# Kernel optimization log

Hardware: AMD Instinct MI355X
Metric: run time of the kernel (lower is better)

Reference implementation:

```python
import jax, jax.numpy as jnp
import numpy as np

N = 50000      # nodes
E = 400000     # edges (before self-loops)
IN = 128       # input feature dim
HID = 32       # out_channels per head
HEADS = 12
NC = 2         # num_classes
SLOPE = 0.2    # GATv2 leaky_relu negative slope


def setup_inputs() -> dict:
    key = jax.random.key(0)
    ks = jax.random.split(key, 24)
    f32 = jnp.float32
    def nrm(k, shape, s=0.1):
        return jax.random.normal(k, shape, dtype=f32) * s
    inp = {}
    inp["x"] = jax.random.normal(ks[0], (N, IN), dtype=f32)
    inp["edge_index"] = jax.random.randint(ks[1], (2, E), 0, N, dtype=jnp.int32)
    # GATv2 layer 0: in=IN, layer 1: in=HID; both heads=HEADS, out=HID, concat=False
    dims = [IN, HID]
    i = 2
    for l, d in enumerate(dims):
        inp[f"Wl{l}"] = nrm(ks[i], (d, HEADS * HID)); i += 1
        inp[f"bl{l}"] = jnp.zeros((HEADS * HID,), f32)
        inp[f"Wr{l}"] = nrm(ks[i], (d, HEADS * HID)); i += 1
        inp[f"br{l}"] = jnp.zeros((HEADS * HID,), f32)
        inp[f"att{l}"] = nrm(ks[i], (HEADS, HID)); i += 1
        inp[f"bias{l}"] = jnp.zeros((HID,), f32)
    # output GATv2Conv(HID, NC): heads=1, concat=True
    inp["Wlo"] = nrm(ks[i], (HID, NC)); i += 1
    inp["blo"] = jnp.zeros((NC,), f32)
    inp["Wro"] = nrm(ks[i], (HID, NC)); i += 1
    inp["bro"] = jnp.zeros((NC,), f32)
    inp["atto"] = nrm(ks[i], (1, NC)); i += 1
    inp["biaso"] = jnp.zeros((NC,), f32)
    return inp


def gatv2_conv(x, src, dst, Wl, bl, Wr, br, att, bias, heads, out_ch, concat):
    """PyG GATv2Conv (share_weights=False, self-loops pre-appended, eval mode)."""
    n = x.shape[0]
    xl = (x @ Wl + bl).reshape(n, heads, out_ch)   # source transform
    xr = (x @ Wr + br).reshape(n, heads, out_ch)   # target transform
    # per-edge attention: e_ij = att . leaky_relu(xl_j + xr_i)
    h = jax.nn.leaky_relu(xl[src] + xr[dst], SLOPE)            # [E, H, C]
    logits = jnp.einsum('ehc,hc->eh', h, att)                   # [E, H]
    # segment softmax over incoming edges per destination node
    m = jax.ops.segment_max(logits, dst, num_segments=n)        # [N, H]
    a = jnp.exp(logits - m[dst])
    denom = jax.ops.segment_sum(a, dst, num_segments=n)         # [N, H]
    alpha = a / (denom[dst] + 1e-16)                            # [E, H]
    out = jax.ops.segment_sum(xl[src] * alpha[..., None], dst, num_segments=n)
    out = out.reshape(n, heads * out_ch) if concat else out.mean(axis=1)
    return out + bias


def reference(x, edge_index, Wl0, bl0, Wr0, br0, att0, bias0,
              Wl1, bl1, Wr1, br1, att1, bias1,
              Wlo, blo, Wro, bro, atto, biaso):
    n = x.shape[0]
    loop = jnp.arange(n, dtype=edge_index.dtype)
    src = jnp.concatenate([edge_index[0], loop])  # add self-loops (PyG default)
    dst = jnp.concatenate([edge_index[1], loop])
    h = gatv2_conv(x, src, dst, Wl0, bl0, Wr0, br0, att0, bias0, HEADS, HID, False)
    h = jax.nn.elu(h)
    h = gatv2_conv(h, src, dst, Wl1, bl1, Wr1, br1, att1, bias1, HEADS, HID, False)
    h = jax.nn.elu(h)
    out = gatv2_conv(h, src, dst, Wlo, blo, Wro, bro, atto, biaso, 1, NC, True)
    return out
```

## Files before the change

### kernel.cpp

```cpp
#include <hip/hip_runtime.h>
#include <hip/hip_fp16.h>
#include <math.h>

#define IN_DIM 128
#define HID 32
#define HEADS 12
#define FDIM (HEADS*HID)
#define SLOPE 0.2f
#define LOG2E 1.44269504f

typedef __attribute__((ext_vector_type(8))) short short8;
typedef __attribute__((ext_vector_type(4))) float float4v;
typedef __attribute__((ext_vector_type(4))) float f32x4;
typedef _Float16 hv2 __attribute__((ext_vector_type(2)));

__device__ __forceinline__ float dot2acc(hv2 a, hv2 b, float c) {
#if __has_builtin(__builtin_amdgcn_fdot2)
    return __builtin_amdgcn_fdot2(a, b, c, false);
#else
    return c + (float)a.x * (float)b.x + (float)a.y * (float)b.y;
#endif
}

__device__ __forceinline__ float exp2h(float x) {
#if __has_builtin(__builtin_amdgcn_exp2f)
    return __builtin_amdgcn_exp2f(x);
#else
    return exp2f(x);
#endif
}

__device__ __forceinline__ float fma_mix_lo(hv2 x, float a, float c) {
    float d;
    asm("v_fma_mix_f32 %0, %1, %2, %3 op_sel_hi:[1,0,0]"
        : "=v"(d) : "v"(x), "v"(a), "v"(c));
    return d;
}
__device__ __forceinline__ float fma_mix_hi(hv2 x, float a, float c) {
    float d;
    asm("v_fma_mix_f32 %0, %1, %2, %3 op_sel:[1,0,0] op_sel_hi:[1,0,0]"
        : "=v"(d) : "v"(x), "v"(a), "v"(c));
    return d;
}

__device__ __forceinline__ void async_cp16(const void* g, void* l) {
    __builtin_amdgcn_global_load_lds(
        (const __attribute__((address_space(1))) void*)g,
        (__attribute__((address_space(3))) void*)l, 16, 0, 0);
}


__global__ __launch_bounds__(256) void scan_partial_kernel(const int* __restrict__ cnt,
                                                           int* __restrict__ partials, int n) {
    int i = blockIdx.x * 256 + threadIdx.x;
    int v = (i < n) ? cnt[i] + 1 : 0;
#pragma unroll
    for (int off = 1; off < 64; off <<= 1) v += __shfl_xor(v, off);
    __shared__ int sh[4];
    if ((threadIdx.x & 63) == 0) sh[threadIdx.x >> 6] = v;
    __syncthreads();
    if (threadIdx.x == 0) partials[blockIdx.x] = sh[0] + sh[1] + sh[2] + sh[3];
}

__global__ __launch_bounds__(256) void scan_final_kernel(const int* __restrict__ cnt,
                                                         const int* __restrict__ partials,
                                                         int* __restrict__ start,
                                                         int* __restrict__ cursor,
                                                         int* __restrict__ srcs,
                                                         int* __restrict__ srcsOff, int n) {
    __shared__ int sh[256];
    __shared__ int ps[4];
    int t = threadIdx.x;
    int pv = 0;
    for (int j = t; j < blockIdx.x; j += 256) pv += partials[j];
#pragma unroll
    for (int off = 1; off < 64; off <<= 1) pv += __shfl_xor(pv, off);
    if ((t & 63) == 0) ps[t >> 6] = pv;

    int i = blockIdx.x * 256 + t;
    int v = (i < n) ? cnt[i] + 1 : 0;
    sh[t] = v;
    __syncthreads();
    int base = ps[0] + ps[1] + ps[2] + ps[3];
    for (int off = 1; off < 256; off <<= 1) {
        int u = (t >= off) ? sh[t - off] : 0;
        __syncthreads();
        sh[t] += u;
        __syncthreads();
    }
    int ex = sh[t] - v + base;
    if (i < n) {
        start[i] = ex;
        cursor[i] = ex;
        int slot = ex + v - 1;
        srcs[slot] = i;
        srcsOff[slot] = i * (FDIM * 2);
        if (i == n - 1) start[n] = ex + v;
    }
}

__global__ void scatter_kernel(const int* __restrict__ src, const int* __restrict__ dst,
                               int* __restrict__ cursor, int* __restrict__ srcs,
                               int* __restrict__ srcsOff, int E) {
    int e = blockIdx.x * blockDim.x + threadIdx.x;
    if (e < E) {
        int d = dst[e];
        int pos = atomicAdd(&cursor[d], 1);
        int s = src[e];
        srcs[pos] = s;
        srcsOff[pos] = s * (FDIM * 2);
    }
}


__device__ __forceinline__ unsigned int bf16_rne(float f) {
    unsigned int u = __float_as_uint(f);
    return (u + 0x7FFFu + ((u >> 16) & 1u)) >> 16;
}


__global__ void prep_conv(const float* __restrict__ x, short* __restrict__ Ah,
                          short* __restrict__ Al, int total4, int convBlocks,
                          const float* __restrict__ Wl0, const float* __restrict__ Wr0,
                          const float* __restrict__ Wl1, const float* __restrict__ Wr1,
                          const float* __restrict__ a0, const float* __restrict__ a1,
                          short* __restrict__ Bl0h, short* __restrict__ Bl0l,
                          short* __restrict__ Br0h, short* __restrict__ Br0l,
                          short* __restrict__ Bl1h, short* __restrict__ Bl1l,
                          short* __restrict__ Br1h, short* __restrict__ Br1l,
                          _Float16* __restrict__ attH,
                          const int* __restrict__ edst, int* __restrict__ cnt, int E) {
    if (blockIdx.x < (unsigned)convBlocks) {
        int i = blockIdx.x * 256 + threadIdx.x;
        if (i >= total4) return;
        float4 v = ((const float4*)x)[i];
        float fs[4] = {v.x, v.y, v.z, v.w};
        unsigned int hb[4], lb[4];
#pragma unroll
        for (int t = 0; t < 4; t++) {
            hb[t] = bf16_rne(fs[t]);
            lb[t] = bf16_rne(fs[t] - __uint_as_float(hb[t] << 16));
        }
        uint2 hp, lp;
        hp.x = hb[0] | (hb[1] << 16); hp.y = hb[2] | (hb[3] << 16);
        lp.x = lb[0] | (lb[1] << 16); lp.y = lb[2] | (lb[3] << 16);
        ((uint2*)Ah)[i] = hp;
        ((uint2*)Al)[i] = lp;
        return;
    }
    if (blockIdx.x < (unsigned)(convBlocks + 243)) {
        int idx = (blockIdx.x - convBlocks) * 256 + threadIdx.x;
        if (idx < 49152) {
            int k = idx / 384, n = idx - k * 384;
            float w1 = Wl0[idx], w2 = Wr0[idx];
            unsigned int h1 = bf16_rne(w1);
            unsigned int l1 = bf16_rne(w1 - __uint_as_float(h1 << 16));
            unsigned int h2 = bf16_rne(w2);
            unsigned int l2 = bf16_rne(w2 - __uint_as_float(h2 << 16));
            Bl0h[n * 128 + k] = (short)h1;  Bl0l[n * 128 + k] = (short)l1;
            Br0h[n * 128 + k] = (short)h2;  Br0l[n * 128 + k] = (short)l2;
        } else if (idx < 61440) {
            int i2 = idx - 49152;
            int k = i2 / 384, n = i2 - k * 384;
            float w1 = Wl1[i2], w2 = Wr1[i2];
            unsigned int h1 = bf16_rne(w1);
            unsigned int l1 = bf16_rne(w1 - __uint_as_float(h1 << 16));
            unsigned int h2 = bf16_rne(w2);
            unsigned int l2 = bf16_rne(w2 - __uint_as_float(h2 << 16));
            Bl1h[n * 32 + k] = (short)h1;  Bl1l[n * 32 + k] = (short)l1;
            Br1h[n * 32 + k] = (short)h2;  Br1l[n * 32 + k] = (short)l2;
        } else if (idx < 62208) {
            int i2 = idx - 61440;
            attH[i2] = (_Float16)(((i2 < 384) ? a0[i2] : a1[i2 - 384]) * LOG2E);
        }
        return;
    }
    int e = (blockIdx.x - convBlocks - 243) * 256 + threadIdx.x;
    if (e < E) atomicAdd(&cnt[edst[e]], 1);
}


__global__ __launch_bounds__(256) void gemm_pair_async(
    const short* __restrict__ Ahi, const short* __restrict__ Alo,
    const short* __restrict__ B1h, const short* __restrict__ B1l,
    const float* __restrict__ bias1, __half* __restrict__ C1,
    const short* __restrict__ B2h, const short* __restrict__ B2l,
    const float* __restrict__ bias2, __half* __restrict__ C2,
    int M, int K, int nwg) {
    __shared__ __align__(16) unsigned char smem[32768];
    int tid = threadIdx.x;
    int lane = tid & 63;
    int wave = tid >> 6;
    int wm = wave & 1, wn = wave >> 1;

    int bid = blockIdx.x;
    int q8 = nwg >> 3, r8 = nwg & 7;
    int xcd = bid & 7, within = bid >> 3;
    int wgid = (xcd < r8 ? xcd * (q8 + 1) : r8 * (q8 + 1) + (xcd - r8) * q8) + within;
    int bx = wgid / 6;
    int by = wgid - bx * 6;

    int rowBase = bx * 128;
    bool second = by >= 3;
    int colBase = (by - (second ? 3 : 0)) * 128;
    const short* Bh  = second ? B2h : B1h;
    const short* Bl  = second ? B2l : B1l;
    const float* bias = second ? bias2 : bias1;
    __half*      C    = second ? C2 : C1;

    const short8* AsHi = (const short8*)smem;
    const short8* AsLo = (const short8*)(smem + 8192);
    const short8* BsHi = (const short8*)(smem + 16384);
    const short8* BsLo = (const short8*)(smem + 24576);

    const short* gsrc[8];
    void* ldst[8];
#pragma unroll
    for (int q = 0; q < 8; q++) {
        int t  = (q & 1) * 4 + wave;
        int rc = t * 16 + (lane & 15);
        int ko = (lane >> 4) * 8;
        const short* base = (q < 2) ? Ahi : (q < 4) ? Alo : (q < 6) ? Bh : Bl;
        int rb = (q < 4) ? rowBase : colBase;
        gsrc[q] = base + (long)(rb + rc) * K + ko;
        ldst[q] = (void*)(smem + q * 4096 + wave * 1024);
    }

    float4v acc[4][4];
#pragma unroll
    for (int i = 0; i < 4; i++)
#pragma unroll
        for (int j = 0; j < 4; j++) acc[i][j] = (float4v){0.f, 0.f, 0.f, 0.f};

    for (int kt = 0; kt < K; kt += 32) {
#pragma unroll
        for (int q = 0; q < 8; q++) {
            async_cp16(gsrc[q], ldst[q]);
            gsrc[q] += 32;
        }
        __syncthreads();

        short8 ah[4], al[4], bh[4], blv[4];
#pragma unroll
        for (int i = 0; i < 4; i++) {
            ah[i]  = AsHi[(wm * 4 + i) * 64 + lane];
            al[i]  = AsLo[(wm * 4 + i) * 64 + lane];
            bh[i]  = BsHi[(wn * 4 + i) * 64 + lane];
            blv[i] = BsLo[(wn * 4 + i) * 64 + lane];
        }
#pragma unroll
        for (int i = 0; i < 4; i++)
#pragma unroll
            for (int j = 0; j < 4; j++) {
                acc[i][j] = __builtin_amdgcn_mfma_f32_16x16x32_bf16(ah[i], bh[j],  acc[i][j], 0, 0, 0);
                acc[i][j] = __builtin_amdgcn_mfma_f32_16x16x32_bf16(ah[i], blv[j], acc[i][j], 0, 0, 0);
                acc[i][j] = __builtin_amdgcn_mfma_f32_16x16x32_bf16(al[i], bh[j],  acc[i][j], 0, 0, 0);
            }
        __syncthreads();
    }

    float* Ct = (float*)smem;
    int cq = lane >> 4, cn = lane & 15;
#pragma unroll
    for (int pp = 0; pp < 4; pp++) {
        int ph = pp >> 1, rr = pp & 1;
        if (wm == ph) {
#pragma unroll
            for (int ii = 0; ii < 2; ii++) {
                int i = 2 * rr + ii;
#pragma unroll
                for (int j = 0; j < 4; j++) {
                    int lrb = ii * 16 + cq * 4;
                    int lc = wn * 64 + j * 16 + cn;
#pragma unroll
                    for (int r = 0; r < 4; r++)
                        Ct[(lrb + r) * 132 + lc] = acc[i][j][r];
                }
            }
        }
        __syncthreads();
#pragma unroll
        for (int k = 0; k < 2; k++) {
            int o = k * 256 + tid;
            int lrb = o >> 4;
            int oc = (o & 15) << 3;
            int gr = rowBase + ph * 64 + rr * 32 + lrb;
            if (gr < M) {
                float4 f0 = *(float4*)&Ct[lrb * 132 + oc];
                float4 f1 = *(float4*)&Ct[lrb * 132 + oc + 4];
                int gc = colBase + oc;
                float4 b0 = *(const float4*)(bias + gc);
                float4 b1 = *(const float4*)(bias + gc + 4);
                __half2 p0 = __floats2half2_rn(f0.x + b0.x, f0.y + b0.y);
                __half2 p1 = __floats2half2_rn(f0.z + b0.z, f0.w + b0.w);
                __half2 p2 = __floats2half2_rn(f1.x + b1.x, f1.y + b1.y);
                __half2 p3 = __floats2half2_rn(f1.z + b1.z, f1.w + b1.w);
                uint4 ov;
                ov.x = *(unsigned int*)&p0;
                ov.y = *(unsigned int*)&p1;
                ov.z = *(unsigned int*)&p2;
                ov.w = *(unsigned int*)&p3;
                *(uint4*)(C + (size_t)gr * FDIM + gc) = ov;
            }
        }
        __syncthreads();
    }
}


__global__ __launch_bounds__(64) void agg_kernel(const __half* __restrict__ xl,
                                                 const __half* __restrict__ xr,
                                                 const _Float16* __restrict__ att_h,
                                                 const float* __restrict__ bias,
                                                 const int* __restrict__ start,
                                                 const int* __restrict__ srcsOff,
                                                 short* __restrict__ houtHi,
                                                 short* __restrict__ houtLo,
                                                 const float* __restrict__ Wl,
                                                 const float* __restrict__ bl,
                                                 const float* __restrict__ Wr,
                                                 const float* __restrict__ br,
                                                 float* __restrict__ xloB,
                                                 float* __restrict__ xroB, int N) {
    int node = blockIdx.x;
    if (node >= N) return;
    int lane = threadIdx.x & 63;
    int hl = lane & 31;
    int half_ = lane >> 5;
    int cb = hl << 3;

    long nodeOff = (long)node * (FDIM * 2);
    hv2 xr2[6], at2[6];
    f32x4 acc[3];
    float s[3];
#pragma unroll
    for (int c = 0; c < 3; c++) {
        uint2 ur = *(const uint2*)((const char*)xr + nodeOff + c * 256 + cb);
        xr2[2*c]   = __builtin_bit_cast(hv2, ur.x);
        xr2[2*c+1] = __builtin_bit_cast(hv2, ur.y);
        uint2 ua = *(const uint2*)((const char*)att_h + c * 256 + cb);
        at2[2*c]   = __builtin_bit_cast(hv2, ua.x);
        at2[2*c+1] = __builtin_bit_cast(hv2, ua.y);
        acc[c] = (f32x4){0.f, 0.f, 0.f, 0.f};
        s[c] = 0.f;
    }
    const hv2 sl2 = {(_Float16)SLOPE, (_Float16)SLOPE};
    const char* xlb = (const char*)xl + cb;

    int e0 = start[node], e1 = start[node + 1];
    int b = e0;

    int offA0 = 0, offA1 = 0;
    if (b + 4 <= e1) {
        offA0 = srcsOff[b + half_];
        offA1 = srcsOff[b + 2 + half_];
    }
    for (; b + 4 <= e1; b += 4) {
        int offN0 = srcsOff[b + 4 + half_];
        int offN1 = srcsOff[b + 6 + half_];
        hv2 xa[2][6];
        {
            const char* base0 = xlb + (long)offA0;
            uint2 u0 = *(const uint2*)(base0);
            uint2 u1 = *(const uint2*)(base0 + 256);
            uint2 u2 = *(const uint2*)(base0 + 512);
            xa[0][0] = __builtin_bit_cast(hv2, u0.x); xa[0][1] = __builtin_bit_cast(hv2, u0.y);
            xa[0][2] = __builtin_bit_cast(hv2, u1.x); xa[0][3] = __builtin_bit_cast(hv2, u1.y);
            xa[0][4] = __builtin_bit_cast(hv2, u2.x); xa[0][5] = __builtin_bit_cast(hv2, u2.y);
            const char* base1 = xlb + (long)offA1;
            uint2 v0 = *(const uint2*)(base1);
            uint2 v1 = *(const uint2*)(base1 + 256);
            uint2 v2 = *(const uint2*)(base1 + 512);
            xa[1][0] = __builtin_bit_cast(hv2, v0.x); xa[1][1] = __builtin_bit_cast(hv2, v0.y);
            xa[1][2] = __builtin_bit_cast(hv2, v1.x); xa[1][3] = __builtin_bit_cast(hv2, v1.y);
            xa[1][4] = __builtin_bit_cast(hv2, v2.x); xa[1][5] = __builtin_bit_cast(hv2, v2.y);
        }
#pragma unroll
        for (int p = 0; p < 2; p++) {
            float pc[3];
#pragma unroll
            for (int c = 0; c < 3; c++) {
                hv2 t0 = xa[p][2*c]   + xr2[2*c];
                hv2 t1 = xa[p][2*c+1] + xr2[2*c+1];
                t0 = __builtin_elementwise_max(t0, t0 * sl2);
                t1 = __builtin_elementwise_max(t1, t1 * sl2);
                pc[c] = dot2acc(t1, at2[2*c+1], dot2acc(t0, at2[2*c], 0.f));
            }
#pragma unroll
            for (int st = 1; st <= 4; st <<= 1) {
                pc[0] += __shfl_xor(pc[0], st);
                pc[1] += __shfl_xor(pc[1], st);
                pc[2] += __shfl_xor(pc[2], st);
            }
#pragma unroll
            for (int c = 0; c < 3; c++) {
                float a = exp2h(pc[c]);
                s[c] += a;
                acc[c].x = fma_mix_lo(xa[p][2*c],   a, acc[c].x);
                acc[c].y = fma_mix_hi(xa[p][2*c],   a, acc[c].y);
                acc[c].z = fma_mix_lo(xa[p][2*c+1], a, acc[c].z);
                acc[c].w = fma_mix_hi(xa[p][2*c+1], a, acc[c].w);
            }
        }
        offA0 = offN0;
        offA1 = offN1;
    }

    if (b < e1) {
        hv2 xa[2][6];
        float mask[2];
#pragma unroll
        for (int p = 0; p < 2; p++) {
            int myIdx = b + p * 2 + half_;
            int ic = min(myIdx, e1 - 1);
            mask[p] = (myIdx < e1) ? 0.f : -1e30f;
            const char* base = xlb + (long)srcsOff[ic];
            uint2 u0 = *(const uint2*)(base);
            uint2 u1 = *(const uint2*)(base + 256);
            uint2 u2 = *(const uint2*)(base + 512);
            xa[p][0] = __builtin_bit_cast(hv2, u0.x); xa[p][1] = __builtin_bit_cast(hv2, u0.y);
            xa[p][2] = __builtin_bit_cast(hv2, u1.x); xa[p][3] = __builtin_bit_cast(hv2, u1.y);
            xa[p][4] = __builtin_bit_cast(hv2, u2.x); xa[p][5] = __builtin_bit_cast(hv2, u2.y);
        }
#pragma unroll
        for (int p = 0; p < 2; p++) {
            float pc[3];
#pragma unroll
            for (int c = 0; c < 3; c++) {
                hv2 t0 = xa[p][2*c]   + xr2[2*c];
                hv2 t1 = xa[p][2*c+1] + xr2[2*c+1];
                t0 = __builtin_elementwise_max(t0, t0 * sl2);
                t1 = __builtin_elementwise_max(t1, t1 * sl2);
                pc[c] = dot2acc(t1, at2[2*c+1], dot2acc(t0, at2[2*c], 0.f));
            }
#pragma unroll
            for (int st = 1; st <= 4; st <<= 1) {
                pc[0] += __shfl_xor(pc[0], st);
                pc[1] += __shfl_xor(pc[1], st);
                pc[2] += __shfl_xor(pc[2], st);
            }
#pragma unroll
            for (int c = 0; c < 3; c++) {
                float a = exp2h(pc[c] + mask[p]);
                s[c] += a;
                acc[c].x = fma_mix_lo(xa[p][2*c],   a, acc[c].x);
                acc[c].y = fma_mix_hi(xa[p][2*c],   a, acc[c].y);
                acc[c].z = fma_mix_lo(xa[p][2*c+1], a, acc[c].z);
                acc[c].w = fma_mix_hi(xa[p][2*c+1], a, acc[c].w);
            }
        }
    }

#pragma unroll
    for (int c = 0; c < 3; c++) {
        acc[c].x += __shfl_xor(acc[c].x, 32);
        acc[c].y += __shfl_xor(acc[c].y, 32);
        acc[c].z += __shfl_xor(acc[c].z, 32);
        acc[c].w += __shfl_xor(acc[c].w, 32);
        s[c] += __shfl_xor(s[c], 32);
    }
    f32x4 v[3];
#pragma unroll
    for (int c = 0; c < 3; c++) {
        float inv = 1.f / (s[c] + 1e-16f);
        f32x4 iv = {inv, inv, inv, inv};
        v[c] = acc[c] * iv;
    }
#pragma unroll
    for (int st = 8; st <= 16; st <<= 1) {
#pragma unroll
        for (int c = 0; c < 3; c++) {
            v[c].x += __shfl_xor(v[c].x, st);
            v[c].y += __shfl_xor(v[c].y, st);
            v[c].z += __shfl_xor(v[c].z, st);
            v[c].w += __shfl_xor(v[c].w, st);
        }
    }
    if (lane < 8) {
        f32x4 b4 = *(const f32x4*)(bias + (hl << 2));
        f32x4 o = (v[0] + v[1] + v[2]) * (f32x4){1.f/12.f, 1.f/12.f, 1.f/12.f, 1.f/12.f} + b4;
        o.x = o.x > 0.f ? o.x : expm1f(o.x);
        o.y = o.y > 0.f ? o.y : expm1f(o.y);
        o.z = o.z > 0.f ? o.z : expm1f(o.z);
        o.w = o.w > 0.f ? o.w : expm1f(o.w);
        if (houtHi) {
            float fs[4] = {o.x, o.y, o.z, o.w};
            unsigned int hb[4], lb[4];
#pragma unroll
            for (int t = 0; t < 4; t++) {
                hb[t] = bf16_rne(fs[t]);
                lb[t] = bf16_rne(fs[t] - __uint_as_float(hb[t] << 16));
            }
            uint2 hp, lp;
            hp.x = hb[0] | (hb[1] << 16); hp.y = hb[2] | (hb[3] << 16);
            lp.x = lb[0] | (lb[1] << 16); lp.y = lb[2] | (lb[3] << 16);
            *(uint2*)(houtHi + (size_t)node * 32 + (hl << 2)) = hp;
            *(uint2*)(houtLo + (size_t)node * 32 + (hl << 2)) = lp;
        }
        if (Wl) {
            f32x4 wl0 = *(const f32x4*)(Wl + (hl << 3));
            f32x4 wl1 = *(const f32x4*)(Wl + (hl << 3) + 4);
            f32x4 wr0 = *(const f32x4*)(Wr + (hl << 3));
            f32x4 wr1 = *(const f32x4*)(Wr + (hl << 3) + 4);
            float l0 = o.x * wl0.x + o.y * wl0.z + o.z * wl1.x + o.w * wl1.z;
            float l1 = o.x * wl0.y + o.y * wl0.w + o.z * wl1.y + o.w * wl1.w;
            float r0 = o.x * wr0.x + o.y * wr0.z + o.z * wr1.x + o.w * wr1.z;
            float r1 = o.x * wr0.y + o.y * wr0.w + o.z * wr1.y + o.w * wr1.w;
#pragma unroll
            for (int st = 1; st <= 4; st <<= 1) {
                l0 += __shfl_xor(l0, st); l1 += __shfl_xor(l1, st);
                r0 += __shfl_xor(r0, st); r1 += __shfl_xor(r1, st);
            }
            if (hl == 0) {
                xloB[2 * node]     = l0 + bl[0];
                xloB[2 * node + 1] = l1 + bl[1];
                xroB[2 * node]     = r0 + br[0];
                xroB[2 * node + 1] = r1 + br[1];
            }
        }
    }
}


__global__ __launch_bounds__(256) void out_agg_kernel(const float* __restrict__ xlo,
                                                      const float* __restrict__ xro,
                                                      const float* __restrict__ atto,
                                                      const float* __restrict__ biaso,
                                                      const int* __restrict__ start,
                                                      const int* __restrict__ srcs,
                                                      float* __restrict__ out, int N) {
    int g = (blockIdx.x * blockDim.x + threadIdx.x) >> 3;
    int j = threadIdx.x & 7;
    if (g >= N) return;
    float a0 = atto[0] * LOG2E, a1 = atto[1] * LOG2E;
    float xr0 = xro[2 * g], xr1 = xro[2 * g + 1];
    float s = 0.f, acc0 = 0.f, acc1 = 0.f;
    int e0 = start[g], e1 = start[g + 1];
    for (int idx = e0 + j; idx < e1; idx += 8) {
        int jj = srcs[idx];
        float x0 = xlo[2 * jj], x1 = xlo[2 * jj + 1];
        float t0 = x0 + xr0, t1 = x1 + xr1;
        t0 = fmaxf(t0, SLOPE * t0);
        t1 = fmaxf(t1, SLOPE * t1);
        float a = exp2h(a0 * t0 + a1 * t1);
        s += a;
        acc0 = fmaf(a, x0, acc0);
        acc1 = fmaf(a, x1, acc1);
    }
#pragma unroll
    for (int st = 1; st <= 4; st <<= 1) {
        s    += __shfl_xor(s, st);
        acc0 += __shfl_xor(acc0, st);
        acc1 += __shfl_xor(acc1, st);
    }
    if (j == 0) {
        float inv = 1.0f / (s + 1e-16f);
        out[2 * g]     = acc0 * inv + biaso[0];
        out[2 * g + 1] = acc1 * inv + biaso[1];
    }
}


extern "C" void kernel_launch(void* const* d_in, const int* in_sizes, int n_in,
                              void* d_out, int out_size, void* d_ws, size_t ws_size,
                              hipStream_t stream) {
    const float* x    = (const float*)d_in[0];
    const int*   ei   = (const int*)d_in[1];
    const float* Wl0  = (const float*)d_in[2];
    const float* bl0  = (const float*)d_in[3];
    const float* Wr0  = (const float*)d_in[4];
    const float* br0  = (const float*)d_in[5];
    const float* att0 = (const float*)d_in[6];
    const float* bias0= (const float*)d_in[7];
    const float* Wl1  = (const float*)d_in[8];
    const float* bl1  = (const float*)d_in[9];
    const float* Wr1  = (const float*)d_in[10];
    const float* br1  = (const float*)d_in[11];
    const float* att1 = (const float*)d_in[12];
    const float* bias1= (const float*)d_in[13];
    const float* Wlo  = (const float*)d_in[14];
    const float* blo  = (const float*)d_in[15];
    const float* Wro  = (const float*)d_in[16];
    const float* bro  = (const float*)d_in[17];
    const float* atto = (const float*)d_in[18];
    const float* biaso= (const float*)d_in[19];

    const int N = in_sizes[0] / IN_DIM;
    const int E = in_sizes[1] / 2;

    char* ws = (char*)d_ws;
    size_t off = 0;
    auto take = [&](size_t bytes) -> char* {
        char* p = ws + off;
        off += (bytes + 255) & ~(size_t)255;
        return p;
    };
    __half* xlf = (__half*)take((size_t)N * FDIM * 2);
    __half* xrf = (__half*)take((size_t)N * FDIM * 2);
    float* xloB = (float*)take((size_t)N * 2 * 4);
    float* xroB = (float*)take((size_t)N * 2 * 4);
    int* cnt    = (int*)take((size_t)N * 4);
    int* startA = (int*)take((size_t)(N + 1) * 4);
    int* cursor = (int*)take((size_t)N * 4);
    int* srcs   = (int*)take((size_t)(E + N) * 4);
    int* srcsOff= (int*)take((size_t)(E + N) * 4);
    int  nb     = (N + 255) / 256;
    int* partials = (int*)take((size_t)nb * 4);
    short* Bl0h = (short*)take((size_t)FDIM * IN_DIM * 2);
    short* Bl0l = (short*)take((size_t)FDIM * IN_DIM * 2);
    short* Br0h = (short*)take((size_t)FDIM * IN_DIM * 2);
    short* Br0l = (short*)take((size_t)FDIM * IN_DIM * 2);
    short* Bl1h = (short*)take((size_t)FDIM * HID * 2);
    short* Bl1l = (short*)take((size_t)FDIM * HID * 2);
    short* Br1h = (short*)take((size_t)FDIM * HID * 2);
    short* Br1l = (short*)take((size_t)FDIM * HID * 2);
    short* xh   = (short*)take((size_t)N * IN_DIM * 2);
    short* xlo_ = (short*)take((size_t)N * IN_DIM * 2);
    short* h0h  = (short*)take((size_t)N * HID * 2);
    short* h0l  = (short*)take((size_t)N * HID * 2);
    _Float16* attH = (_Float16*)take((size_t)768 * 2);
    (void)take(32768);

    const int* esrc = ei;
    const int* edst = ei + E;

    hipMemsetAsync(cnt, 0, (size_t)N * 4, stream);

    int total4 = N * IN_DIM / 4;
    int convBlocks = (total4 + 255) / 256;
    int histBlocks = (E + 255) / 256;
    prep_conv<<<convBlocks + 243 + histBlocks, 256, 0, stream>>>(
        x, xh, xlo_, total4, convBlocks,
        Wl0, Wr0, Wl1, Wr1, att0, att1,
        Bl0h, Bl0l, Br0h, Br0l,
        Bl1h, Bl1l, Br1h, Br1l, attH,
        edst, cnt, E);

    scan_partial_kernel<<<nb, 256, 0, stream>>>(cnt, partials, N);
    scan_final_kernel<<<nb, 256, 0, stream>>>(cnt, partials, startA, cursor, srcs, srcsOff, N);
    scatter_kernel<<<(E + 255) / 256, 256, 0, stream>>>(esrc, edst, cursor, srcs, srcsOff, E);

    int gx = (N + 127) / 128;
    int nwg = gx * 6;
    gemm_pair_async<<<nwg, 256, 0, stream>>>(xh, xlo_, Bl0h, Bl0l, bl0, xlf, Br0h, Br0l, br0, xrf, N, IN_DIM, nwg);
    agg_kernel<<<N, 64, 0, stream>>>(xlf, xrf, attH, bias0, startA, srcsOff,
                                     h0h, h0l, nullptr, nullptr, nullptr, nullptr,
                                     nullptr, nullptr, N);
    gemm_pair_async<<<nwg, 256, 0, stream>>>(h0h, h0l, Bl1h, Bl1l, bl1, xlf, Br1h, Br1l, br1, xrf, N, HID, nwg);
    agg_kernel<<<N, 64, 0, stream>>>(xlf, xrf, attH + 384, bias1, startA, srcsOff,
                                     nullptr, nullptr, Wlo, blo, Wro, bro,
                                     xloB, xroB, N);
    out_agg_kernel<<<((size_t)N * 8 + 255) / 256, 256, 0, stream>>>(xloB, xroB, atto, biaso, startA, srcs, (float*)d_out, N);
}
```

Baseline: 361.3 us.

## Software-pipeline edge gathers with double-buffered feature registers in aggregation loop

Restructures the per-node edge aggregation loop so the xl feature gather for the next group of four edges is issued before computing the current group, using two register buffers that alternate. The separate masked tail path is merged into the main loop by clamping indices and masking every iteration. This aims to hide gather latency behind the attention/accumulate math, at the cost of more live registers, masking work on every iteration, and one wasted gather per node.

```diff
diff --git a/kernel.cpp b/kernel.cpp
--- a/kernel.cpp
+++ b/kernel.cpp
@@ -348,35 +348,32 @@
     const char* xlb = (const char*)xl + cb;
 
     int e0 = start[node], e1 = start[node + 1];
-    int b = e0;
-
-    int offA0 = 0, offA1 = 0;
-    if (b + 4 <= e1) {
-        offA0 = srcsOff[b + half_];
-        offA1 = srcsOff[b + 2 + half_];
-    }
-    for (; b + 4 <= e1; b += 4) {
-        int offN0 = srcsOff[b + 4 + half_];
-        int offN1 = srcsOff[b + 6 + half_];
-        hv2 xa[2][6];
-        {
-            const char* base0 = xlb + (long)offA0;
-            uint2 u0 = *(const uint2*)(base0);
-            uint2 u1 = *(const uint2*)(base0 + 256);
-            uint2 u2 = *(const uint2*)(base0 + 512);
-            xa[0][0] = __builtin_bit_cast(hv2, u0.x); xa[0][1] = __builtin_bit_cast(hv2, u0.y);
-            xa[0][2] = __builtin_bit_cast(hv2, u1.x); xa[0][3] = __builtin_bit_cast(hv2, u1.y);
-            xa[0][4] = __builtin_bit_cast(hv2, u2.x); xa[0][5] = __builtin_bit_cast(hv2, u2.y);
-            const char* base1 = xlb + (long)offA1;
-            uint2 v0 = *(const uint2*)(base1);
-            uint2 v1 = *(const uint2*)(base1 + 256);
-            uint2 v2 = *(const uint2*)(base1 + 512);
-            xa[1][0] = __builtin_bit_cast(hv2, v0.x); xa[1][1] = __builtin_bit_cast(hv2, v0.y);
-            xa[1][2] = __builtin_bit_cast(hv2, v1.x); xa[1][3] = __builtin_bit_cast(hv2, v1.y);
-            xa[1][4] = __builtin_bit_cast(hv2, v2.x); xa[1][5] = __builtin_bit_cast(hv2, v2.y);
-        }
+    int e1m1 = e1 - 1;
+
+    auto prepOff = [&](int b, int (&off)[2]) {
 #pragma unroll
         for (int p = 0; p < 2; p++) {
+            int ic = min(b + p * 2 + half_, e1m1);
+            off[p] = srcsOff[ic];
+        }
+    };
+    auto gather = [&](const int (&off)[2], hv2 (&xa)[2][6]) {
+#pragma unroll
+        for (int p = 0; p < 2; p++) {
+            const char* b = xlb + (long)off[p];
+            uint2 u0 = *(const uint2*)(b);
+            uint2 u1 = *(const uint2*)(b + 256);
+            uint2 u2 = *(const uint2*)(b + 512);
+            xa[p][0] = __builtin_bit_cast(hv2, u0.x); xa[p][1] = __builtin_bit_cast(hv2, u0.y);
+            xa[p][2] = __builtin_bit_cast(hv2, u1.x); xa[p][3] = __builtin_bit_cast(hv2, u1.y);
+            xa[p][4] = __builtin_bit_cast(hv2, u2.x); xa[p][5] = __builtin_bit_cast(hv2, u2.y);
+        }
+    };
+    auto compute = [&](int b, const hv2 (&xa)[2][6]) {
+#pragma unroll
+        for (int p = 0; p < 2; p++) {
+            int myIdx = b + p * 2 + half_;
+            float mask = (myIdx < e1) ? 0.f : -1e30f;
             float pc[3];
 #pragma unroll
             for (int c = 0; c < 3; c++) {
@@ -394,7 +391,7 @@
             }
 #pragma unroll
             for (int c = 0; c < 3; c++) {
-                float a = exp2h(pc[c]);
+                float a = exp2h(pc[c] + mask);
                 s[c] += a;
                 acc[c].x = fma_mix_lo(xa[p][2*c],   a, acc[c].x);
                 acc[c].y = fma_mix_hi(xa[p][2*c],   a, acc[c].y);
@@ -402,53 +399,27 @@
                 acc[c].w = fma_mix_hi(xa[p][2*c+1], a, acc[c].w);
             }
         }
-        offA0 = offN0;
-        offA1 = offN1;
-    }
-
-    if (b < e1) {
-        hv2 xa[2][6];
-        float mask[2];
-#pragma unroll
-        for (int p = 0; p < 2; p++) {
-            int myIdx = b + p * 2 + half_;
-            int ic = min(myIdx, e1 - 1);
-            mask[p] = (myIdx < e1) ? 0.f : -1e30f;
-            const char* base = xlb + (long)srcsOff[ic];
-            uint2 u0 = *(const uint2*)(base);
-            uint2 u1 = *(const uint2*)(base + 256);
-            uint2 u2 = *(const uint2*)(base + 512);
-            xa[p][0] = __builtin_bit_cast(hv2, u0.x); xa[p][1] = __builtin_bit_cast(hv2, u0.y);
-            xa[p][2] = __builtin_bit_cast(hv2, u1.x); xa[p][3] = __builtin_bit_cast(hv2, u1.y);
-            xa[p][4] = __builtin_bit_cast(hv2, u2.x); xa[p][5] = __builtin_bit_cast(hv2, u2.y);
-        }
-#pragma unroll
-        for (int p = 0; p < 2; p++) {
-            float pc[3];
-#pragma unroll
-            for (int c = 0; c < 3; c++) {
-                hv2 t0 = xa[p][2*c]   + xr2[2*c];
-                hv2 t1 = xa[p][2*c+1] + xr2[2*c+1];
-                t0 = __builtin_elementwise_max(t0, t0 * sl2);
-                t1 = __builtin_elementwise_max(t1, t1 * sl2);
-                pc[c] = dot2acc(t1, at2[2*c+1], dot2acc(t0, at2[2*c], 0.f));
-            }
-#pragma unroll
-            for (int st = 1; st <= 4; st <<= 1) {
-                pc[0] += __shfl_xor(pc[0], st);
-                pc[1] += __shfl_xor(pc[1], st);
-                pc[2] += __shfl_xor(pc[2], st);
-            }
-#pragma unroll
-            for (int c = 0; c < 3; c++) {
-                float a = exp2h(pc[c] + mask[p]);
-                s[c] += a;
-                acc[c].x = fma_mix_lo(xa[p][2*c],   a, acc[c].x);
-                acc[c].y = fma_mix_hi(xa[p][2*c],   a, acc[c].y);
-                acc[c].z = fma_mix_lo(xa[p][2*c+1], a, acc[c].z);
-                acc[c].w = fma_mix_hi(xa[p][2*c+1], a, acc[c].w);
-            }
-        }
+    };
+
+    int offA[2], offB[2];
+    hv2 xaA[2][6], xaB[2][6];
+    int base = e0;
+    prepOff(base, offA);
+    gather(offA, xaA);
+    prepOff(base + 4, offB);
+
+    while (true) {
+        gather(offB, xaB);
+        prepOff(base + 8, offA);
+        compute(base, xaA);
+        base += 4;
+        if (base >= e1) break;
+
+        gather(offA, xaA);
+        prepOff(base + 8, offB);
+        compute(base, xaB);
+        base += 4;
+        if (base >= e1) break;
     }
 
 #pragma unroll
```

Measured after the change: 365.6 us. Within noise of the previous version (+1.2%).
